# Kernel optimization log

Hardware: AMD Instinct MI355X
Metric: run time of the kernel (lower is better)

## Reference

```python
import jax, jax.numpy as jnp
import numpy as np

N = 100000
E = 3200000
F = 256          # feature_size
NUM_CLASSES = 40
HEADS = 2
C = 16 // HEADS  # out_channels per head = 8


def setup_inputs() -> dict:
    key = jax.random.key(0)
    ks = jax.random.split(key, 16)
    s = 0.05
    return {
        "x": jax.random.normal(ks[0], (N, F), dtype=jnp.float32),
        "y": jax.random.randint(ks[1], (N,), 0, NUM_CLASSES, dtype=jnp.int32),
        "edge_index": jax.random.randint(ks[2], (2, E), 0, N, dtype=jnp.int32),
        "label_mask": jax.random.bernoulli(ks[3], 0.5, (N,)),
        "emb": jax.random.normal(ks[4], (NUM_CLASSES, F), dtype=jnp.float32) * s,
        "Wq": jax.random.normal(ks[5], (F, HEADS * C), dtype=jnp.float32) * s,
        "bq": jnp.zeros((HEADS * C,), dtype=jnp.float32),
        "Wk": jax.random.normal(ks[6], (F, HEADS * C), dtype=jnp.float32) * s,
        "bk": jnp.zeros((HEADS * C,), dtype=jnp.float32),
        "Wv": jax.random.normal(ks[7], (F, HEADS * C), dtype=jnp.float32) * s,
        "bv": jnp.zeros((HEADS * C,), dtype=jnp.float32),
        "Wskip": jax.random.normal(ks[8], (F, HEADS * C), dtype=jnp.float32) * s,
        "bskip": jnp.zeros((HEADS * C,), dtype=jnp.float32),
        "Wout": jax.random.normal(ks[9], (HEADS * C, NUM_CLASSES), dtype=jnp.float32) * s,
        "bout": jnp.zeros((NUM_CLASSES,), dtype=jnp.float32),
    }


def reference(x, y, edge_index, label_mask, emb, Wq, bq, Wk, bk, Wv, bv, Wskip, bskip, Wout, bout):
    n = x.shape[0]
    # MaskLabel: masked label embedding added to node features
    h = x + jnp.where(label_mask[:, None], emb[y], 0.0)

    # TransformerConv (concat=True, beta=False, root_weight=True)
    q = (h @ Wq + bq).reshape(n, HEADS, C)
    k = (h @ Wk + bk).reshape(n, HEADS, C)
    v = (h @ Wv + bv).reshape(n, HEADS, C)

    src, dst = edge_index[0], edge_index[1]  # messages flow src -> dst
    # per-edge attention logits [E, HEADS]
    alpha = jnp.einsum('ehc,ehc->eh', q[dst], k[src]) / jnp.sqrt(jnp.float32(C))
    # scatter-softmax over incoming edges of each dst node
    amax = jax.ops.segment_max(alpha, dst, num_segments=n)
    ex = jnp.exp(alpha - amax[dst])
    denom = jax.ops.segment_sum(ex, dst, num_segments=n)
    att = ex / (denom[dst] + 1e-16)
    # weighted scatter-add of values
    msg = v[src] * att[:, :, None]                       # [E, H, C]
    agg = jax.ops.segment_sum(msg, dst, num_segments=n)  # [N, H, C]
    out = agg.reshape(n, HEADS * C) + (h @ Wskip + bskip)

    # final classifier
    return out @ Wout + bout
```

## Files before the change

### kernel.cpp

```cpp
#include <hip/hip_runtime.h>
#include <stdint.h>


constexpr int F_DIM = 256;
constexpr int NC = 40;
constexpr float RSQRT8 = 0.35355339059327373f;

constexpr int SHIFT = 9;
constexpr int NPBKT = 1 << SHIFT;
constexpr int NBLK1 = 512;
constexpr int MAXB1 = 256;
constexpr int DCAP = 32768;

typedef __attribute__((ext_vector_type(8))) short short8;
typedef __attribute__((ext_vector_type(4))) float f32x4;

__device__ __forceinline__ unsigned int bfbits(float f) {
  unsigned int u = __float_as_uint(f);
  return (u + 0x7fffu + ((u >> 16) & 1u)) >> 16;
}
__device__ __forceinline__ float bflo(unsigned int u) { return __uint_as_float(u << 16); }
__device__ __forceinline__ float bfhi(unsigned int u) { return __uint_as_float(u & 0xffff0000u); }

__global__ void detect_mask_kernel(const unsigned char* __restrict__ m, int* __restrict__ flag) {
  __shared__ int any;
  if (threadIdx.x == 0) any = 0;
  __syncthreads();
  int acc = 0;
  for (int i = threadIdx.x; i < 1024; i += blockDim.x)
    acc |= m[i * 4 + 1] | m[i * 4 + 2] | m[i * 4 + 3];
  if (acc) atomicOr(&any, 1);
  __syncthreads();
  if (threadIdx.x == 0) *flag = any ? 0 : 1;
}

__global__ void weight_prep_kernel(const float* __restrict__ Wq, const float* __restrict__ Wk,
                                   const float* __restrict__ Wv, const float* __restrict__ Ws,
                                   ushort* __restrict__ wbf) {
  int i = blockIdx.x * 256 + threadIdx.x;
  if (i >= 64 * 256) return;
  int col = i >> 8, k = i & 255;
  const float* W = (col < 16) ? Wq : (col < 32) ? Wk : (col < 48) ? Wv : Ws;
  wbf[i] = (ushort)bfbits(W[k * 16 + (col & 15)]);
}

__global__ __launch_bounds__(256) void fused_gemm_mfma(
    const float* __restrict__ x, const int* __restrict__ y,
    const unsigned char* __restrict__ maskraw, const int* __restrict__ flag,
    const float* __restrict__ emb, const ushort* __restrict__ wbf,
    const float* __restrict__ bq, const float* __restrict__ bk,
    const float* __restrict__ bv, const float* __restrict__ bs,
    float* __restrict__ qout, float* __restrict__ skipout,
    ushort* __restrict__ kvout, int n)
{
  __shared__ ushort wlds[64][272];
  const int tid = threadIdx.x;

  {
    const uint4* wsrc = (const uint4*)wbf;
    for (int i = tid; i < 2048; i += 256) {
      int col = i >> 5, seg = i & 31;
      uint4 d = wsrc[i];
      *(uint4*)&wlds[col][seg * 8] = d;
    }
  }
  __syncthreads();

  const int w = tid >> 6, lane = tid & 63;
  const int r15 = lane & 15, grp = lane >> 4;
  const int nbase = blockIdx.x * 64 + w * 16;
  int row = min(nbase + r15, n - 1);
  const int flg = *flag;
  bool msk = flg ? (((const int*)maskraw)[row] != 0) : (maskraw[row] != 0);
  int cls = y[row];

  f32x4 acc[4];
#pragma unroll
  for (int ct = 0; ct < 4; ++ct)
#pragma unroll
    for (int j = 0; j < 4; ++j) acc[ct][j] = 0.f;

  const float4* xp = (const float4*)(x + (size_t)row * F_DIM + grp * 8);
  const float4* ep = (const float4*)(emb + (size_t)cls * F_DIM + grp * 8);

  for (int ks = 0; ks < 8; ++ks) {
    float4 xa = xp[ks * 8];
    float4 xb = xp[ks * 8 + 1];
    if (msk) {
      float4 ea = ep[ks * 8], eb = ep[ks * 8 + 1];
      xa.x += ea.x; xa.y += ea.y; xa.z += ea.z; xa.w += ea.w;
      xb.x += eb.x; xb.y += eb.y; xb.z += eb.z; xb.w += eb.w;
    }
    short8 a;
    a[0] = (short)bfbits(xa.x); a[1] = (short)bfbits(xa.y);
    a[2] = (short)bfbits(xa.z); a[3] = (short)bfbits(xa.w);
    a[4] = (short)bfbits(xb.x); a[5] = (short)bfbits(xb.y);
    a[6] = (short)bfbits(xb.z); a[7] = (short)bfbits(xb.w);
    const int kofs = ks * 32 + grp * 8;
#pragma unroll
    for (int ct = 0; ct < 4; ++ct) {
      short8 b = *(const short8*)&wlds[ct * 16 + r15][kofs];
      acc[ct] = __builtin_amdgcn_mfma_f32_16x16x32_bf16(a, b, acc[ct], 0, 0, 0);
    }
  }

  const float bqv = bq[r15], bkv = bk[r15], bvv = bv[r15], bsv = bs[r15];
#pragma unroll
  for (int r = 0; r < 4; ++r) {
    int nr = nbase + grp * 4 + r;
    if (nr < n) {
      qout[(size_t)nr * 16 + r15] = (acc[0][r] + bqv) * RSQRT8;
      kvout[(size_t)nr * 32 + r15] = (ushort)bfbits(acc[1][r] + bkv);
      kvout[(size_t)nr * 32 + 16 + r15] = (ushort)bfbits(acc[2][r] + bvv);
      skipout[(size_t)nr * 16 + r15] = acc[3][r] + bsv;
    }
  }
}

__global__ __launch_bounds__(256) void bucket_hist_kernel(
    const int* __restrict__ dstA, int* __restrict__ M, int etot, int chunk, int nb1)
{
  __shared__ int h[MAXB1];
  const int tid = threadIdx.x, b = blockIdx.x;
  for (int i = tid; i < nb1; i += 256) h[i] = 0;
  __syncthreads();
  int s = b * chunk, e = min(etot, s + chunk);
  for (int i = s + tid; i < e; i += 256) atomicAdd(&h[dstA[i] >> SHIFT], 1);
  __syncthreads();
  for (int i = tid; i < nb1; i += 256) M[i * NBLK1 + b] = h[i];
}

__global__ __launch_bounds__(NBLK1) void col_scan_kernel(
    int* __restrict__ M, int* __restrict__ tot)
{
  __shared__ int s[NBLK1];
  const int t = threadIdx.x, k = blockIdx.x;
  int v = M[k * NBLK1 + t];
  s[t] = v;
  __syncthreads();
  for (int off = 1; off < NBLK1; off <<= 1) {
    int tt = (t >= off) ? s[t - off] : 0;
    __syncthreads();
    s[t] += tt;
    __syncthreads();
  }
  M[k * NBLK1 + t] = s[t] - v;
  if (t == NBLK1 - 1) tot[k] = s[t];
}

__global__ __launch_bounds__(256) void tot_scan_kernel(
    const int* __restrict__ tot, int* __restrict__ bucket_base, int nb1, int etot)
{
  __shared__ int s[256];
  const int t = threadIdx.x;
  int v = (t < nb1) ? tot[t] : 0;
  s[t] = v;
  __syncthreads();
  for (int off = 1; off < 256; off <<= 1) {
    int tt = (t >= off) ? s[t - off] : 0;
    __syncthreads();
    s[t] += tt;
    __syncthreads();
  }
  if (t < nb1) bucket_base[t] = s[t] - v;
  if (t == 0) bucket_base[nb1] = etot;
}

__global__ __launch_bounds__(256) void bucket_scatter_kernel(
    const int* __restrict__ srcA, const int* __restrict__ dstA,
    const int* __restrict__ M, const int* __restrict__ bucket_base,
    unsigned int* __restrict__ bucketed, int etot, int chunk, int nb1)
{
  __shared__ int c[MAXB1];
  const int tid = threadIdx.x, b = blockIdx.x;
  for (int i = tid; i < nb1; i += 256) c[i] = M[i * NBLK1 + b] + bucket_base[i];
  __syncthreads();
  int s = b * chunk, e = min(etot, s + chunk);
  for (int i = s + tid; i < e; i += 256) {
    int d = dstA[i];
    int k = d >> SHIFT;
    int pos = atomicAdd(&c[k], 1);
    bucketed[pos] = ((unsigned)(d & (NPBKT - 1)) << 17) | (unsigned)srcA[i];
  }
}

__global__ __launch_bounds__(1024) void csr_build_kernel(
    unsigned int* __restrict__ bucketed, const int* __restrict__ bucket_base,
    int* __restrict__ offsets, int* __restrict__ counts, int n)
{
  extern __shared__ unsigned int sedge[];
  __shared__ int h[NPBKT], sc[NPBKT], cur[NPBKT];
  const int tid = threadIdx.x, k = blockIdx.x;
  const int base = bucket_base[k];
  int cnt = bucket_base[k + 1] - base;
  if (cnt > DCAP) cnt = DCAP;
  if (tid < NPBKT) h[tid] = 0;
  __syncthreads();
  for (int i = tid; i < cnt; i += 1024) {
    unsigned p = bucketed[base + i];
    sedge[i] = p;
    atomicAdd(&h[p >> 17], 1);
  }
  __syncthreads();
  int v = (tid < NPBKT) ? h[tid] : 0;
  if (tid < NPBKT) sc[tid] = v;
  __syncthreads();
  for (int off = 1; off < NPBKT; off <<= 1) {
    int t = 0;
    if (tid < NPBKT && tid >= off) t = sc[tid - off];
    __syncthreads();
    if (tid < NPBKT) sc[tid] += t;
    __syncthreads();
  }
  if (tid < NPBKT) {
    int excl = sc[tid] - v;
    cur[tid] = excl;
    int node = (k << SHIFT) + tid;
    if (node < n) { offsets[node] = base + excl; counts[node] = v; }
  }
  __syncthreads();
  for (int i = tid; i < cnt; i += 1024) {
    unsigned p = sedge[i];
    int pos = atomicAdd(&cur[p >> 17], 1);
    bucketed[base + pos] = p & 0x1FFFFu;
  }
}

__global__ __launch_bounds__(256) void edge_attn_kernel(
    const int* __restrict__ csr, const int* __restrict__ offsets,
    const int* __restrict__ counts, const float* __restrict__ q,
    const float* __restrict__ skip, const unsigned int* __restrict__ kv,
    const float* __restrict__ Wout, const float* __restrict__ bout,
    float* __restrict__ out, int n)
{
  int wave = (blockIdx.x * blockDim.x + threadIdx.x) >> 6;
  int lane = threadIdx.x & 63;
  if (wave >= n) return;
  int dst = __builtin_amdgcn_readfirstlane(wave);

  int start = offsets[dst];
  int cnt = counts[dst];

  float qv[16];
#pragma unroll
  for (int o = 0; o < 16; ++o) qv[o] = q[(size_t)dst * 16 + o];

  float es0 = 0.f, es1 = 0.f;
  float acc[16];
#pragma unroll
  for (int o = 0; o < 16; ++o) acc[o] = 0.f;

  for (int b = 0; b < cnt; b += 64) {
    int e = b + lane;
    if (e < cnt) {
      int s = csr[start + e];
      const uint4* kvp = (const uint4*)(kv + (size_t)s * 16);
      uint4 kA = kvp[0], kB = kvp[1], vA = kvp[2], vB = kvp[3];
      float kf[16], vf[16];
      kf[0] = bflo(kA.x); kf[1] = bfhi(kA.x); kf[2] = bflo(kA.y); kf[3] = bfhi(kA.y);
      kf[4] = bflo(kA.z); kf[5] = bfhi(kA.z); kf[6] = bflo(kA.w); kf[7] = bfhi(kA.w);
      kf[8] = bflo(kB.x); kf[9] = bfhi(kB.x); kf[10] = bflo(kB.y); kf[11] = bfhi(kB.y);
      kf[12] = bflo(kB.z); kf[13] = bfhi(kB.z); kf[14] = bflo(kB.w); kf[15] = bfhi(kB.w);
      vf[0] = bflo(vA.x); vf[1] = bfhi(vA.x); vf[2] = bflo(vA.y); vf[3] = bfhi(vA.y);
      vf[4] = bflo(vA.z); vf[5] = bfhi(vA.z); vf[6] = bflo(vA.w); vf[7] = bfhi(vA.w);
      vf[8] = bflo(vB.x); vf[9] = bfhi(vB.x); vf[10] = bflo(vB.y); vf[11] = bfhi(vB.y);
      vf[12] = bflo(vB.z); vf[13] = bfhi(vB.z); vf[14] = bflo(vB.w); vf[15] = bfhi(vB.w);
      float a0 = 0.f, a1 = 0.f;
#pragma unroll
      for (int c2 = 0; c2 < 8; ++c2) {
        a0 = fmaf(qv[c2], kf[c2], a0);
        a1 = fmaf(qv[8 + c2], kf[8 + c2], a1);
      }
      float e0 = __expf(a0), e1 = __expf(a1);
      es0 += e0; es1 += e1;
#pragma unroll
      for (int c2 = 0; c2 < 8; ++c2) {
        acc[c2] = fmaf(e0, vf[c2], acc[c2]);
        acc[8 + c2] = fmaf(e1, vf[8 + c2], acc[8 + c2]);
      }
    }
  }

#pragma unroll
  for (int m = 1; m <= 32; m <<= 1) {
    es0 += __shfl_xor(es0, m, 64);
    es1 += __shfl_xor(es1, m, 64);
#pragma unroll
    for (int o = 0; o < 16; ++o) acc[o] += __shfl_xor(acc[o], m, 64);
  }

  float d0 = es0 + 1e-16f, d1 = es1 + 1e-16f;
  float out16[16];
#pragma unroll
  for (int o = 0; o < 8; ++o)  out16[o] = acc[o] / d0 + skip[(size_t)dst * 16 + o];
#pragma unroll
  for (int o = 8; o < 16; ++o) out16[o] = acc[o] / d1 + skip[(size_t)dst * 16 + o];

  if (lane < NC) {
    float r = bout[lane];
#pragma unroll
    for (int c2 = 0; c2 < 16; ++c2) r = fmaf(out16[c2], Wout[c2 * NC + lane], r);
    out[(size_t)dst * NC + lane] = r;
  }
}

extern "C" void kernel_launch(void* const* d_in, const int* in_sizes, int n_in,
                              void* d_out, int out_size, void* d_ws, size_t ws_size,
                              hipStream_t stream) {
  const float* x = (const float*)d_in[0];
  const int* y = (const int*)d_in[1];
  const int* ei = (const int*)d_in[2];
  const unsigned char* mask = (const unsigned char*)d_in[3];
  const float* emb = (const float*)d_in[4];
  const float* Wq = (const float*)d_in[5];
  const float* bq = (const float*)d_in[6];
  const float* Wk = (const float*)d_in[7];
  const float* bk = (const float*)d_in[8];
  const float* Wv = (const float*)d_in[9];
  const float* bv = (const float*)d_in[10];
  const float* Ws = (const float*)d_in[11];
  const float* bs = (const float*)d_in[12];
  const float* Wout = (const float*)d_in[13];
  const float* bout = (const float*)d_in[14];

  const int n = in_sizes[1];
  const int etot = in_sizes[2] / 2;
  const int nb1 = (n + NPBKT - 1) >> SHIFT;
  const int chunk = (etot + NBLK1 - 1) / NBLK1;

  char* w = (char*)d_ws;
  size_t off = 0;
  auto alloc = [&](size_t bytes) -> void* {
    off = (off + 255) & ~(size_t)255;
    void* p = w + off;
    off += bytes;
    return p;
  };
  int* flag = (int*)alloc(sizeof(int));
  ushort* wbf = (ushort*)alloc((size_t)64 * 256 * sizeof(ushort));
  float* qbuf = (float*)alloc((size_t)n * 16 * sizeof(float));
  float* skipbuf = (float*)alloc((size_t)n * 16 * sizeof(float));
  ushort* kvbuf = (ushort*)alloc((size_t)n * 32 * sizeof(ushort));
  int* counts = (int*)alloc((size_t)n * sizeof(int));
  int* offsets = (int*)alloc((size_t)n * sizeof(int));
  int* M = (int*)alloc((size_t)MAXB1 * NBLK1 * sizeof(int));
  int* tot = (int*)alloc((size_t)MAXB1 * sizeof(int));
  int* bucket_base = (int*)alloc(((size_t)nb1 + 1) * sizeof(int));
  unsigned int* bucketed = (unsigned int*)alloc((size_t)etot * sizeof(unsigned int));

  detect_mask_kernel<<<1, 256, 0, stream>>>(mask, flag);
  weight_prep_kernel<<<64, 256, 0, stream>>>(Wq, Wk, Wv, Ws, wbf);
  fused_gemm_mfma<<<(n + 63) / 64, 256, 0, stream>>>(
      x, y, mask, flag, emb, wbf, bq, bk, bv, bs, qbuf, skipbuf, kvbuf, n);
  bucket_hist_kernel<<<NBLK1, 256, 0, stream>>>(ei + etot, M, etot, chunk, nb1);
  col_scan_kernel<<<nb1, NBLK1, 0, stream>>>(M, tot);
  tot_scan_kernel<<<1, 256, 0, stream>>>(tot, bucket_base, nb1, etot);
  bucket_scatter_kernel<<<NBLK1, 256, 0, stream>>>(ei, ei + etot, M, bucket_base, bucketed, etot, chunk, nb1);
  csr_build_kernel<<<nb1, 1024, DCAP * sizeof(unsigned int), stream>>>(
      bucketed, bucket_base, offsets, counts, n);
  edge_attn_kernel<<<(n + 3) / 4, 256, 0, stream>>>(
      (const int*)bucketed, offsets, counts, qbuf, skipbuf,
      (const unsigned int*)kvbuf, Wout, bout, (float*)d_out, n);
}
```

Before: 410.1 us.

## Process each destination node with 16 lanes instead of a full wavefront

The edge attention kernel now assigns 16 lanes per destination node (four nodes per wavefront) instead of 64. With an average in-degree near 32, most of the 64 lanes sat idle. The change shortens the shuffle reduction to four steps, vectorises the q and skip loads, and replaces the divisions with one reciprocal. Each lane now writes up to three output classes. Dst is no longer wave-uniform, so its loads become per-lane, and high-degree nodes take more loop iterations.

```diff
diff --git a/kernel.cpp b/kernel.cpp
--- a/kernel.cpp
+++ b/kernel.cpp
@@ -233,74 +233,93 @@
     const float* __restrict__ Wout, const float* __restrict__ bout,
     float* __restrict__ out, int n)
 {
-  int wave = (blockIdx.x * blockDim.x + threadIdx.x) >> 6;
-  int lane = threadIdx.x & 63;
-  if (wave >= n) return;
-  int dst = __builtin_amdgcn_readfirstlane(wave);
-
-  int start = offsets[dst];
-  int cnt = counts[dst];
+  const int dst = (blockIdx.x * blockDim.x + threadIdx.x) >> 4;
+  const int l16 = threadIdx.x & 15;
+  if (dst >= n) return;
+
+  const int start = offsets[dst];
+  const int cnt = counts[dst];
 
   float qv[16];
-#pragma unroll
-  for (int o = 0; o < 16; ++o) qv[o] = q[(size_t)dst * 16 + o];
+  {
+    const float4* qp = (const float4*)(q + (size_t)dst * 16);
+    float4 q0 = qp[0], q1 = qp[1], q2 = qp[2], q3 = qp[3];
+    qv[0] = q0.x; qv[1] = q0.y; qv[2] = q0.z; qv[3] = q0.w;
+    qv[4] = q1.x; qv[5] = q1.y; qv[6] = q1.z; qv[7] = q1.w;
+    qv[8] = q2.x; qv[9] = q2.y; qv[10] = q2.z; qv[11] = q2.w;
+    qv[12] = q3.x; qv[13] = q3.y; qv[14] = q3.z; qv[15] = q3.w;
+  }
 
   float es0 = 0.f, es1 = 0.f;
   float acc[16];
 #pragma unroll
   for (int o = 0; o < 16; ++o) acc[o] = 0.f;
 
-  for (int b = 0; b < cnt; b += 64) {
-    int e = b + lane;
-    if (e < cnt) {
-      int s = csr[start + e];
-      const uint4* kvp = (const uint4*)(kv + (size_t)s * 16);
-      uint4 kA = kvp[0], kB = kvp[1], vA = kvp[2], vB = kvp[3];
-      float kf[16], vf[16];
-      kf[0] = bflo(kA.x); kf[1] = bfhi(kA.x); kf[2] = bflo(kA.y); kf[3] = bfhi(kA.y);
-      kf[4] = bflo(kA.z); kf[5] = bfhi(kA.z); kf[6] = bflo(kA.w); kf[7] = bfhi(kA.w);
-      kf[8] = bflo(kB.x); kf[9] = bfhi(kB.x); kf[10] = bflo(kB.y); kf[11] = bfhi(kB.y);
-      kf[12] = bflo(kB.z); kf[13] = bfhi(kB.z); kf[14] = bflo(kB.w); kf[15] = bfhi(kB.w);
-      vf[0] = bflo(vA.x); vf[1] = bfhi(vA.x); vf[2] = bflo(vA.y); vf[3] = bfhi(vA.y);
-      vf[4] = bflo(vA.z); vf[5] = bfhi(vA.z); vf[6] = bflo(vA.w); vf[7] = bfhi(vA.w);
-      vf[8] = bflo(vB.x); vf[9] = bfhi(vB.x); vf[10] = bflo(vB.y); vf[11] = bfhi(vB.y);
-      vf[12] = bflo(vB.z); vf[13] = bfhi(vB.z); vf[14] = bflo(vB.w); vf[15] = bfhi(vB.w);
-      float a0 = 0.f, a1 = 0.f;
-#pragma unroll
-      for (int c2 = 0; c2 < 8; ++c2) {
-        a0 = fmaf(qv[c2], kf[c2], a0);
-        a1 = fmaf(qv[8 + c2], kf[8 + c2], a1);
-      }
-      float e0 = __expf(a0), e1 = __expf(a1);
-      es0 += e0; es1 += e1;
-#pragma unroll
-      for (int c2 = 0; c2 < 8; ++c2) {
-        acc[c2] = fmaf(e0, vf[c2], acc[c2]);
-        acc[8 + c2] = fmaf(e1, vf[8 + c2], acc[8 + c2]);
-      }
-    }
-  }
-
-#pragma unroll
-  for (int m = 1; m <= 32; m <<= 1) {
+  for (int e = l16; e < cnt; e += 16) {
+    int s = csr[start + e];
+    const uint4* kvp = (const uint4*)(kv + (size_t)s * 16);
+    uint4 kA = kvp[0], kB = kvp[1], vA = kvp[2], vB = kvp[3];
+    float kf[16], vf[16];
+    kf[0] = bflo(kA.x); kf[1] = bfhi(kA.x); kf[2] = bflo(kA.y); kf[3] = bfhi(kA.y);
+    kf[4] = bflo(kA.z); kf[5] = bfhi(kA.z); kf[6] = bflo(kA.w); kf[7] = bfhi(kA.w);
+    kf[8] = bflo(kB.x); kf[9] = bfhi(kB.x); kf[10] = bflo(kB.y); kf[11] = bfhi(kB.y);
+    kf[12] = bflo(kB.z); kf[13] = bfhi(kB.z); kf[14] = bflo(kB.w); kf[15] = bfhi(kB.w);
+    vf[0] = bflo(vA.x); vf[1] = bfhi(vA.x); vf[2] = bflo(vA.y); vf[3] = bfhi(vA.y);
+    vf[4] = bflo(vA.z); vf[5] = bfhi(vA.z); vf[6] = bflo(vA.w); vf[7] = bfhi(vA.w);
+    vf[8] = bflo(vB.x); vf[9] = bfhi(vB.x); vf[10] = bflo(vB.y); vf[11] = bfhi(vB.y);
+    vf[12] = bflo(vB.z); vf[13] = bfhi(vB.z); vf[14] = bflo(vB.w); vf[15] = bfhi(vB.w);
+    float a0 = 0.f, a1 = 0.f;
+#pragma unroll
+    for (int c2 = 0; c2 < 8; ++c2) {
+      a0 = fmaf(qv[c2], kf[c2], a0);
+      a1 = fmaf(qv[8 + c2], kf[8 + c2], a1);
+    }
+    float e0 = __expf(a0), e1 = __expf(a1);
+    es0 += e0; es1 += e1;
+#pragma unroll
+    for (int c2 = 0; c2 < 8; ++c2) {
+      acc[c2] = fmaf(e0, vf[c2], acc[c2]);
+      acc[8 + c2] = fmaf(e1, vf[8 + c2], acc[8 + c2]);
+    }
+  }
+
+#pragma unroll
+  for (int m = 1; m <= 8; m <<= 1) {
     es0 += __shfl_xor(es0, m, 64);
     es1 += __shfl_xor(es1, m, 64);
 #pragma unroll
     for (int o = 0; o < 16; ++o) acc[o] += __shfl_xor(acc[o], m, 64);
   }
 
-  float d0 = es0 + 1e-16f, d1 = es1 + 1e-16f;
+  const float i0 = 1.0f / (es0 + 1e-16f);
+  const float i1 = 1.0f / (es1 + 1e-16f);
   float out16[16];
-#pragma unroll
-  for (int o = 0; o < 8; ++o)  out16[o] = acc[o] / d0 + skip[(size_t)dst * 16 + o];
-#pragma unroll
-  for (int o = 8; o < 16; ++o) out16[o] = acc[o] / d1 + skip[(size_t)dst * 16 + o];
-
-  if (lane < NC) {
-    float r = bout[lane];
-#pragma unroll
-    for (int c2 = 0; c2 < 16; ++c2) r = fmaf(out16[c2], Wout[c2 * NC + lane], r);
-    out[(size_t)dst * NC + lane] = r;
+  {
+    const float4* sp = (const float4*)(skip + (size_t)dst * 16);
+    float4 s0 = sp[0], s1 = sp[1], s2 = sp[2], s3 = sp[3];
+    out16[0] = fmaf(acc[0], i0, s0.x);  out16[1] = fmaf(acc[1], i0, s0.y);
+    out16[2] = fmaf(acc[2], i0, s0.z);  out16[3] = fmaf(acc[3], i0, s0.w);
+    out16[4] = fmaf(acc[4], i0, s1.x);  out16[5] = fmaf(acc[5], i0, s1.y);
+    out16[6] = fmaf(acc[6], i0, s1.z);  out16[7] = fmaf(acc[7], i0, s1.w);
+    out16[8] = fmaf(acc[8], i1, s2.x);  out16[9] = fmaf(acc[9], i1, s2.y);
+    out16[10] = fmaf(acc[10], i1, s2.z); out16[11] = fmaf(acc[11], i1, s2.w);
+    out16[12] = fmaf(acc[12], i1, s3.x); out16[13] = fmaf(acc[13], i1, s3.y);
+    out16[14] = fmaf(acc[14], i1, s3.z); out16[15] = fmaf(acc[15], i1, s3.w);
+  }
+
+  float r0 = bout[l16], r1 = bout[l16 + 16];
+#pragma unroll
+  for (int c2 = 0; c2 < 16; ++c2) {
+    r0 = fmaf(out16[c2], Wout[c2 * NC + l16], r0);
+    r1 = fmaf(out16[c2], Wout[c2 * NC + l16 + 16], r1);
+  }
+  out[(size_t)dst * NC + l16] = r0;
+  out[(size_t)dst * NC + l16 + 16] = r1;
+  if (l16 < 8) {
+    float r2 = bout[l16 + 32];
+#pragma unroll
+    for (int c2 = 0; c2 < 16; ++c2) r2 = fmaf(out16[c2], Wout[c2 * NC + l16 + 32], r2);
+    out[(size_t)dst * NC + l16 + 32] = r2;
   }
 }
 
@@ -358,7 +377,7 @@
   bucket_scatter_kernel<<<NBLK1, 256, 0, stream>>>(ei, ei + etot, M, bucket_base, bucketed, etot, chunk, nb1);
   csr_build_kernel<<<nb1, 1024, DCAP * sizeof(unsigned int), stream>>>(
       bucketed, bucket_base, offsets, counts, n);
-  edge_attn_kernel<<<(n + 3) / 4, 256, 0, stream>>>(
+  edge_attn_kernel<<<(n + 15) / 16, 256, 0, stream>>>(
       (const int*)bucketed, offsets, counts, qbuf, skipbuf,
       (const unsigned int*)kvbuf, Wout, bout, (float*)d_out, n);
 }
```

Measured after the change: 338.3 us. 1.21x faster.
